# Performance work log

Measured on AMD Instinct MI355X. Metric: run time of the kernel, lower is better.

Reference implementation:

```python
import jax, jax.numpy as jnp
import numpy as np

EMB = 384
H = 6
D = 64  # head_size = EMB // H
FF = 4 * EMB
B, T = 256, 256
EPS = 1e-5


def layernorm(x, g, b):
    mu = jnp.mean(x, axis=-1, keepdims=True)
    var = jnp.var(x, axis=-1, keepdims=True)
    return (x - mu) * jax.lax.rsqrt(var + EPS) * g + b


def setup_inputs() -> dict:
    key = jax.random.key(0)
    ks = jax.random.split(key, 12)
    s_qkv = 1.0 / np.sqrt(EMB)
    return {
        "x":  jax.random.normal(ks[0], (B, T, EMB), jnp.float32),
        # per-head Q/K/V projections stacked: [EMB, H, D]
        "Wq": jax.random.normal(ks[1], (EMB, H, D), jnp.float32) * s_qkv,
        "Wk": jax.random.normal(ks[2], (EMB, H, D), jnp.float32) * s_qkv,
        "Wv": jax.random.normal(ks[3], (EMB, H, D), jnp.float32) * s_qkv,
        "Wo": jax.random.normal(ks[4], (EMB, EMB), jnp.float32) * s_qkv,
        "bo": jnp.zeros((EMB,), jnp.float32),
        "W1": jax.random.normal(ks[5], (EMB, FF), jnp.float32) * s_qkv,
        "b1": jnp.zeros((FF,), jnp.float32),
        "W2": jax.random.normal(ks[6], (FF, EMB), jnp.float32) * (1.0 / np.sqrt(FF)),
        "b2": jnp.zeros((EMB,), jnp.float32),
        "g1": jnp.ones((EMB,), jnp.float32),
        "be1": jnp.zeros((EMB,), jnp.float32),
        "g2": jnp.ones((EMB,), jnp.float32),
        "be2": jnp.zeros((EMB,), jnp.float32),
    }


def reference(x, Wq, Wk, Wv, Wo, bo, W1, b1, W2, b2, g1, be1, g2, be2):
    # pre-LN attention (unmasked encoder block, dropout in eval mode = identity)
    h = layernorm(x, g1, be1)                      # [B,T,C]
    q = jnp.einsum('btc,chd->bhtd', h, Wq)
    k = jnp.einsum('btc,chd->bhtd', h, Wk)
    v = jnp.einsum('btc,chd->bhtd', h, Wv)
    scores = jnp.einsum('bhtd,bhsd->bhts', q, k) * (D ** -0.5)
    attn = jax.nn.softmax(scores, axis=-1)         # [B,H,T,T]
    o = jnp.einsum('bhts,bhsd->bhtd', attn, v)
    o = o.transpose(0, 2, 1, 3).reshape(x.shape[0], x.shape[1], EMB)  # concat heads
    x = x + o @ Wo + bo
    h2 = layernorm(x, g2, be2)
    ff = jax.nn.relu(h2 @ W1 + b1) @ W2 + b2
    return x + ff
```

## Files before the change

### kernel.cpp

```cpp
#include <hip/hip_runtime.h>

typedef __attribute__((ext_vector_type(8))) short bf16x8;
typedef __attribute__((ext_vector_type(4))) float f32x4;
typedef __attribute__((ext_vector_type(4))) unsigned short u16x4;
typedef __attribute__((ext_vector_type(4))) unsigned int u32x4;
typedef __attribute__((ext_vector_type(2))) unsigned int u32x2;

#define DEVFN static __device__ __forceinline__

DEVFN unsigned short f2b(float f) {
  union { float f; unsigned u; } x; x.f = f;
  unsigned r = x.u + 0x7FFFu + ((x.u >> 16) & 1u);
  return (unsigned short)(r >> 16);
}

DEVFN unsigned cvtpk(float lo, float hi) {
  unsigned r;
  asm("v_cvt_pk_bf16_f32 %0, %1, %2" : "=v"(r) : "v"(lo), "v"(hi));
  return r;
}

DEVFN void gll16(const void* g, void* l) {
  __builtin_amdgcn_global_load_lds(
      (const __attribute__((address_space(1))) unsigned int*)g,
      (__attribute__((address_space(3))) unsigned int*)l, 16, 0, 0);
}

#define MFMA16(a, b, c) __builtin_amdgcn_mfma_f32_16x16x32_bf16((a), (b), (c), 0, 0, 0)

__global__ __launch_bounds__(256) void prep_kernel(
    const float* __restrict__ Wq, const float* __restrict__ Wk, const float* __restrict__ Wv,
    const float* __restrict__ Wo, const float* __restrict__ W1, const float* __restrict__ W2,
    short* __restrict__ wqkvT, short* __restrict__ woT,
    short* __restrict__ w1T, short* __restrict__ w2T)
{
  int idx = blockIdx.x * 256 + threadIdx.x;
  if (idx < 442368) {
    int n = idx / 384, kk = idx - n * 384;
    int sec = n / 384, ww = n - sec * 384;
    const float* s = sec == 0 ? Wq : (sec == 1 ? Wk : Wv);
    float sc = (sec == 0) ? 0.125f : 1.0f;
    wqkvT[idx] = (short)f2b(s[kk * 384 + ww] * sc);
  } else if (idx < 589824) {
    int j = idx - 442368;
    int n = j / 384, kk = j - n * 384;
    woT[j] = (short)f2b(Wo[kk * 384 + n]);
  } else if (idx < 1179648) {
    int j = idx - 589824;
    int n = j / 384, kk = j - n * 384;
    w1T[j] = (short)f2b(W1[kk * 1536 + n]);
  } else if (idx < 1769472) {
    int j = idx - 1179648;
    int n = j / 1536, kk = j - n * 1536;
    w2T[j] = (short)f2b(W2[kk * 384 + n]);
  }
}

__global__ __launch_bounds__(256) void ln_kernel(
    const float* __restrict__ x, const float* __restrict__ g, const float* __restrict__ b,
    short* __restrict__ out)
{
  int row = blockIdx.x * 4 + (threadIdx.x >> 6);
  int l = threadIdx.x & 63;
  const float* xr = x + (size_t)row * 384;
  float v[6], s = 0.f, s2 = 0.f;
  #pragma unroll
  for (int i = 0; i < 6; ++i) { v[i] = xr[l + 64 * i]; s += v[i]; s2 += v[i] * v[i]; }
  #pragma unroll
  for (int m = 1; m < 64; m <<= 1) { s += __shfl_xor(s, m); s2 += __shfl_xor(s2, m); }
  float mu = s * (1.f / 384.f);
  float rs = rsqrtf(s2 * (1.f / 384.f) - mu * mu + 1e-5f);
  short* orow = out + (size_t)row * 384;
  #pragma unroll
  for (int i = 0; i < 6; ++i) {
    int c = l + 64 * i;
    orow[c] = (short)f2b((v[i] - mu) * rs * g[c] + b[c]);
  }
}

template<int EPI>
__global__ __launch_bounds__(512) void gemm_bt(
    const short* __restrict__ A, const short* __restrict__ BT,
    int K, int kt, int N, int nx,
    const float* __restrict__ bias, const float* __restrict__ resid,
    float* __restrict__ fout,
    short* __restrict__ qb, short* __restrict__ kb, short* __restrict__ vb)
{
  __shared__ short As[256 * 64];
  __shared__ short Bs[128 * 64];
  const int tid = threadIdx.x;
  const int l = tid & 63, w = tid >> 6;
  const int cl = l & 15, rq = l >> 4;
  const int wr = (w >> 1) * 64, wc = (w & 1) * 64;

  const int nwg = gridDim.x, bid = blockIdx.x;
  const int q8 = nwg >> 3, r8 = nwg & 7;
  const int xcd = bid & 7, ii = bid >> 3;
  const int wg = (xcd < r8) ? xcd * (q8 + 1) + ii : r8 * (q8 + 1) + (xcd - r8) * q8 + ii;
  const int bx = wg % nx, by = wg / nx;

  const int m0 = by * 256, n0 = bx * 128;
  const short* Ab = A + (size_t)m0 * K;
  const short* Bb = BT + (size_t)n0 * K;

  f32x4 acc[4][4] = {};

  for (int ks = 0; ks < kt; ++ks) {
    const int k0 = ks * 64;
    __syncthreads();
    #pragma unroll
    for (int i = 0; i < 4; ++i) {
      int slot = i * 512 + tid;
      int row = slot >> 3, g = slot & 7;
      int gs = g ^ (row & 7);
      gll16(Ab + (size_t)row * K + k0 + gs * 8, &As[slot * 8]);
    }
    #pragma unroll
    for (int i = 0; i < 2; ++i) {
      int slot = i * 512 + tid;
      int row = slot >> 3, g = slot & 7;
      int gs = g ^ (row & 7);
      gll16(Bb + (size_t)row * K + k0 + gs * 8, &Bs[slot * 8]);
    }
    __syncthreads();
    #pragma unroll
    for (int kk = 0; kk < 2; ++kk) {
      bf16x8 af[4], bfr[4];
      #pragma unroll
      for (int m = 0; m < 4; ++m) {
        int row = wr + m * 16 + cl;
        af[m] = *(const bf16x8*)&As[row * 64 + (((kk * 4 + rq) ^ (row & 7)) * 8)];
      }
      #pragma unroll
      for (int n = 0; n < 4; ++n) {
        int row = wc + n * 16 + cl;
        bfr[n] = *(const bf16x8*)&Bs[row * 64 + (((kk * 4 + rq) ^ (row & 7)) * 8)];
      }
      #pragma unroll
      for (int m = 0; m < 4; ++m)
        #pragma unroll
        for (int n = 0; n < 4; ++n)
          acc[m][n] = MFMA16(af[m], bfr[n], acc[m][n]);
    }
  }

  const int gr0 = m0 + wr, gc0 = n0 + wc;
  #pragma unroll
  for (int m = 0; m < 4; ++m) {
    #pragma unroll
    for (int n = 0; n < 4; ++n) {
      int col = gc0 + n * 16 + cl;
      int rbase = gr0 + m * 16 + rq * 4;
      if constexpr (EPI == 0) {
        int sec = col / 384;
        int wcol = col - sec * 384;
        int hh = wcol >> 6, d = wcol & 63;
        int bidx = rbase >> 8, t0 = rbase & 255;
        if (sec == 2) {
          u16x4 pk;
          #pragma unroll
          for (int r = 0; r < 4; ++r) pk[r] = f2b(acc[m][n][r]);
          *(u16x4*)&vb[((size_t)(bidx * 6 + hh) * 64 + d) * 256 + t0] = pk;
        } else {
          short* dst = (sec == 0) ? qb : kb;
          #pragma unroll
          for (int r = 0; r < 4; ++r)
            dst[((size_t)(bidx * 6 + hh) * 256 + t0 + r) * 64 + d] = (short)f2b(acc[m][n][r]);
        }
      } else {
        #pragma unroll
        for (int r = 0; r < 4; ++r) {
          size_t ix = (size_t)(rbase + r) * N + col;
          fout[ix] = acc[m][n][r] + bias[col] + resid[ix];
        }
      }
    }
  }
}

__global__ __launch_bounds__(512, 2) void ff_fused(
    const short* __restrict__ h2,
    const short* __restrict__ w1T,
    const short* __restrict__ w2T,
    const float* __restrict__ b1, const float* __restrict__ b2,
    float* __restrict__ out)
{
  __shared__ short As[128 * 64];
  __shared__ short W1s[128 * 64];
  __shared__ short Acts[128 * 128];
  __shared__ short W2s[384 * 64];
  const int tid = threadIdx.x;
  const int l = tid & 63, w = tid >> 6;
  const int cl = l & 15, rq = l >> 4;
  const int wm = w >> 2, wn = w & 3;
  const int m0 = blockIdx.x * 128;

  f32x4 acc[4][6] = {};

  for (int c = 0; c < 12; ++c) {
    f32x4 aacc[8] = {};
    for (int ks = 0; ks < 6; ++ks) {
      __syncthreads();
      #pragma unroll
      for (int i = 0; i < 2; ++i) {
        int slot = i * 512 + tid;
        int row = slot >> 3, g = slot & 7;
        int gs = g ^ (row & 7);
        gll16(h2 + (size_t)(m0 + row) * 384 + ks * 64 + gs * 8, &As[slot * 8]);
        gll16(w1T + (size_t)(c * 128 + row) * 384 + ks * 64 + gs * 8, &W1s[slot * 8]);
      }
      __syncthreads();
      #pragma unroll
      for (int kk = 0; kk < 2; ++kk) {
        int wrow = w * 16 + cl;
        bf16x8 w1f = *(const bf16x8*)&W1s[wrow * 64 + (((kk * 4 + rq) ^ (wrow & 7)) * 8)];
        #pragma unroll
        for (int m8 = 0; m8 < 8; ++m8) {
          int arow = m8 * 16 + cl;
          bf16x8 hf = *(const bf16x8*)&As[arow * 64 + (((kk * 4 + rq) ^ (arow & 7)) * 8)];
          aacc[m8] = MFMA16(w1f, hf, aacc[m8]);
        }
      }
    }
    f32x4 b1v = *(const f32x4*)&b1[c * 128 + w * 16 + 4 * rq];
    #pragma unroll
    for (int m8 = 0; m8 < 8; ++m8) {
      int row = m8 * 16 + cl;
      int gran = 2 * w + (rq >> 1);
      int off = row * 128 + ((gran ^ (row & 7)) * 8) + ((rq & 1) * 4);
      float v0 = fmaxf(aacc[m8][0] + b1v[0], 0.f);
      float v1 = fmaxf(aacc[m8][1] + b1v[1], 0.f);
      float v2 = fmaxf(aacc[m8][2] + b1v[2], 0.f);
      float v3 = fmaxf(aacc[m8][3] + b1v[3], 0.f);
      u32x2 pw; pw[0] = cvtpk(v0, v1); pw[1] = cvtpk(v2, v3);
      *(u32x2*)&Acts[off] = pw;
    }
    #pragma unroll
    for (int fk = 0; fk < 2; ++fk) {
      __syncthreads();
      #pragma unroll
      for (int i = 0; i < 6; ++i) {
        int slot = i * 512 + tid;
        int row = slot >> 3, g = slot & 7;
        int gs = g ^ (row & 7);
        gll16(w2T + (size_t)row * 1536 + c * 128 + fk * 64 + gs * 8, &W2s[slot * 8]);
      }
      __syncthreads();
      #pragma unroll
      for (int kk = 0; kk < 2; ++kk) {
        bf16x8 af[4], bf[6];
        #pragma unroll
        for (int m = 0; m < 4; ++m) {
          int row = wm * 64 + m * 16 + cl;
          int gran = fk * 8 + kk * 4 + rq;
          af[m] = *(const bf16x8*)&Acts[row * 128 + ((gran ^ (row & 7)) * 8)];
        }
        #pragma unroll
        for (int n = 0; n < 6; ++n) {
          int row = wn * 96 + n * 16 + cl;
          bf[n] = *(const bf16x8*)&W2s[row * 64 + (((kk * 4 + rq) ^ (row & 7)) * 8)];
        }
        #pragma unroll
        for (int m = 0; m < 4; ++m)
          #pragma unroll
          for (int n = 0; n < 6; ++n)
            acc[m][n] = MFMA16(af[m], bf[n], acc[m][n]);
      }
    }
  }
  #pragma unroll
  for (int m = 0; m < 4; ++m) {
    #pragma unroll
    for (int n = 0; n < 6; ++n) {
      int col = wn * 96 + n * 16 + cl;
      int rbase = m0 + wm * 64 + m * 16 + 4 * rq;
      #pragma unroll
      for (int r = 0; r < 4; ++r) {
        size_t ix = (size_t)(rbase + r) * 384 + col;
        out[ix] = acc[m][n][r] + b2[col] + out[ix];
      }
    }
  }
}

__global__ __launch_bounds__(1024) void attn_kernel(
    const short* __restrict__ qg, const short* __restrict__ kg,
    const short* __restrict__ vg, short* __restrict__ og)
{
  __shared__ short Ks[256 * 64];
  __shared__ short Vs[64 * 256];
  const int tid = threadIdx.x;
  const int bh = blockIdx.x;
  const int w = tid >> 6, l = tid & 63;
  const int cl = l & 15, rq = l >> 4;
  const short* kgb = kg + (size_t)bh * 16384;
  const short* vgb = vg + (size_t)bh * 16384;
  #pragma unroll
  for (int i = 0; i < 2; ++i) {
    int slot = i * 1024 + tid;
    int row = slot >> 3, g = slot & 7;
    gll16(kgb + row * 64 + (g ^ (row & 7)) * 8, &Ks[slot * 8]);
  }
  #pragma unroll
  for (int i = 0; i < 2; ++i) {
    int slot = i * 1024 + tid;
    int row = slot >> 5, g = slot & 31;
    int gs = (g & 24) | ((g ^ row) & 7);
    gll16(vgb + row * 256 + gs * 8, &Vs[slot * 8]);
  }
  const int qrow = w * 16 + cl;
  const bf16x8* qp = (const bf16x8*)(qg + ((size_t)bh * 256 + qrow) * 64 + rq * 8);
  bf16x8 qf0 = qp[0], qf1 = qp[4];
  const int b = bh / 6, hh = bh - b * 6;
  __syncthreads();

  f32x4 s[16] = {};
  #pragma unroll
  for (int c = 0; c < 16; ++c) {
    int srow = c * 16 + cl;
    bf16x8 k0 = *(const bf16x8*)&Ks[srow * 64 + ((rq ^ (srow & 7)) * 8)];
    bf16x8 k1 = *(const bf16x8*)&Ks[srow * 64 + (((4 + rq) ^ (srow & 7)) * 8)];
    s[c] = MFMA16(k0, qf0, s[c]);
    s[c] = MFMA16(k1, qf1, s[c]);
  }
  float mr[8];
  #pragma unroll
  for (int c = 0; c < 8; ++c)
    mr[c] = fmaxf(fmaxf(fmaxf(s[2*c][0], s[2*c][1]), fmaxf(s[2*c][2], s[2*c][3])),
                  fmaxf(fmaxf(s[2*c+1][0], s[2*c+1][1]), fmaxf(s[2*c+1][2], s[2*c+1][3])));
  float m = fmaxf(fmaxf(fmaxf(mr[0], mr[1]), fmaxf(mr[2], mr[3])),
                  fmaxf(fmaxf(mr[4], mr[5]), fmaxf(mr[6], mr[7])));
  m = fmaxf(m, __shfl_xor(m, 16));
  m = fmaxf(m, __shfl_xor(m, 32));
  float tc[16];
  #pragma unroll
  for (int c = 0; c < 16; ++c) {
    #pragma unroll
    for (int r = 0; r < 4; ++r) s[c][r] = __expf(s[c][r] - m);
    tc[c] = (s[c][0] + s[c][1]) + (s[c][2] + s[c][3]);
  }
  float t = ((tc[0]+tc[1])+(tc[2]+tc[3])) + ((tc[4]+tc[5])+(tc[6]+tc[7]))
          + ((tc[8]+tc[9])+(tc[10]+tc[11])) + ((tc[12]+tc[13])+(tc[14]+tc[15]));
  t += __shfl_xor(t, 16);
  t += __shfl_xor(t, 32);
  const float inv = 1.f / t;

  f32x4 oacc[4] = {};
  const int idx1 = (((2 * rq) & 3) * 16 + cl) << 2;
  const int idx2 = (((2 * rq + 1) & 3) * 16 + cl) << 2;
  const bool up = rq >= 2;
  #pragma unroll
  for (int ch = 0; ch < 8; ++ch) {
    int X0 = (int)cvtpk(s[2*ch][0], s[2*ch][1]);
    int X1 = (int)cvtpk(s[2*ch][2], s[2*ch][3]);
    int X2 = (int)cvtpk(s[2*ch+1][0], s[2*ch+1][1]);
    int X3 = (int)cvtpk(s[2*ch+1][2], s[2*ch+1][3]);
    int lo0 = __builtin_amdgcn_ds_bpermute(idx1, X0);
    int lo1 = __builtin_amdgcn_ds_bpermute(idx1, X1);
    int hi0 = __builtin_amdgcn_ds_bpermute(idx1, X2);
    int hi1 = __builtin_amdgcn_ds_bpermute(idx1, X3);
    int lo2 = __builtin_amdgcn_ds_bpermute(idx2, X0);
    int lo3 = __builtin_amdgcn_ds_bpermute(idx2, X1);
    int hi2 = __builtin_amdgcn_ds_bpermute(idx2, X2);
    int hi3 = __builtin_amdgcn_ds_bpermute(idx2, X3);
    u32x4 words;
    words[0] = (unsigned)(up ? hi0 : lo0);
    words[1] = (unsigned)(up ? hi1 : lo1);
    words[2] = (unsigned)(up ? hi2 : lo2);
    words[3] = (unsigned)(up ? hi3 : lo3);
    bf16x8 pa = __builtin_bit_cast(bf16x8, words);
    #pragma unroll
    for (int n = 0; n < 4; ++n) {
      int vrow = n * 16 + cl;
      int gg = ch * 4 + rq;
      int gs = (gg & 24) | ((gg ^ vrow) & 7);
      bf16x8 vf = *(const bf16x8*)&Vs[vrow * 256 + gs * 8];
      oacc[n] = MFMA16(pa, vf, oacc[n]);
    }
  }
  float invr[4];
  #pragma unroll
  for (int r = 0; r < 4; ++r) invr[r] = __shfl(inv, 4 * rq + r);
  #pragma unroll
  for (int n = 0; n < 4; ++n) {
    #pragma unroll
    for (int r = 0; r < 4; ++r) {
      int trow = w * 16 + 4 * rq + r;
      og[((size_t)(b * 256 + trow)) * 384 + hh * 64 + n * 16 + cl] =
          (short)f2b(oacc[n][r] * invr[r]);
    }
  }
}

extern "C" void kernel_launch(void* const* d_in, const int* in_sizes, int n_in,
                              void* d_out, int out_size, void* d_ws, size_t ws_size,
                              hipStream_t stream) {
  const float* x   = (const float*)d_in[0];
  const float* Wq  = (const float*)d_in[1];
  const float* Wk  = (const float*)d_in[2];
  const float* Wv  = (const float*)d_in[3];
  const float* Wo  = (const float*)d_in[4];
  const float* bo  = (const float*)d_in[5];
  const float* W1  = (const float*)d_in[6];
  const float* b1  = (const float*)d_in[7];
  const float* W2  = (const float*)d_in[8];
  const float* b2  = (const float*)d_in[9];
  const float* g1  = (const float*)d_in[10];
  const float* be1 = (const float*)d_in[11];
  const float* g2  = (const float*)d_in[12];
  const float* be2 = (const float*)d_in[13];

  char* ws = (char*)d_ws;
  short* wqkvT = (short*)(ws);
  short* woT   = (short*)(ws + 884736);
  short* w1T   = (short*)(ws + 1179648);
  short* w2T   = (short*)(ws + 2359296);
  short* bufA  = (short*)(ws + 3538944);
  short* h  = bufA;
  short* q  = bufA + 25165824;
  short* k  = bufA + 50331648;
  short* v  = bufA + 75497472;
  short* o  = bufA;
  short* h2 = bufA + 25165824;
  float* out = (float*)d_out;

  prep_kernel<<<6912, 256, 0, stream>>>(Wq, Wk, Wv, Wo, W1, W2, wqkvT, woT, w1T, w2T);
  ln_kernel<<<16384, 256, 0, stream>>>(x, g1, be1, h);
  gemm_bt<0><<<9 * 256, 512, 0, stream>>>(h, wqkvT, 384, 6, 1152, 9,
      nullptr, nullptr, nullptr, q, k, v);
  attn_kernel<<<1536, 1024, 0, stream>>>(q, k, v, o);
  gemm_bt<1><<<3 * 256, 512, 0, stream>>>(o, woT, 384, 6, 384, 3,
      bo, x, out, nullptr, nullptr, nullptr);
  ln_kernel<<<16384, 256, 0, stream>>>(out, g2, be2, h2);
  ff_fused<<<512, 512, 0, stream>>>(h2, w1T, w2T, b1, b2, out);
}
```

Baseline: 583.5 us.

## Restructure fused FFN: 64-row tiles, resident activations in LDS, weights from global

```diff
diff --git a/kernel.cpp b/kernel.cpp
--- a/kernel.cpp
+++ b/kernel.cpp
@@ -178,102 +178,92 @@
   }
 }
 
-__global__ __launch_bounds__(512, 2) void ff_fused(
+__global__ __launch_bounds__(512, 4) void ff_fused(
     const short* __restrict__ h2,
     const short* __restrict__ w1T,
     const short* __restrict__ w2T,
     const float* __restrict__ b1, const float* __restrict__ b2,
     float* __restrict__ out)
 {
-  __shared__ short As[128 * 64];
-  __shared__ short W1s[128 * 64];
-  __shared__ short Acts[128 * 128];
-  __shared__ short W2s[384 * 64];
+  __shared__ short As[64 * 384];
+  __shared__ short Acts[64 * 128];
   const int tid = threadIdx.x;
   const int l = tid & 63, w = tid >> 6;
   const int cl = l & 15, rq = l >> 4;
   const int wm = w >> 2, wn = w & 3;
-  const int m0 = blockIdx.x * 128;
-
-  f32x4 acc[4][6] = {};
+  const int m0 = blockIdx.x * 64;
+
+  #pragma unroll
+  for (int i = 0; i < 6; ++i) {
+    int slot = i * 512 + tid;
+    int row = slot / 48, g = slot - row * 48;
+    int gs = (g & 56) | ((g ^ row) & 7);
+    gll16(h2 + (size_t)(m0 + row) * 384 + gs * 8, &As[slot * 8]);
+  }
+  __syncthreads();
+
+  f32x4 acc[2][6] = {};
 
   for (int c = 0; c < 12; ++c) {
-    f32x4 aacc[8] = {};
+    f32x4 aacc[4] = {};
+    const short* w1p = w1T + (size_t)(c * 128 + w * 16 + cl) * 384;
+    #pragma unroll
     for (int ks = 0; ks < 6; ++ks) {
-      __syncthreads();
-      #pragma unroll
-      for (int i = 0; i < 2; ++i) {
-        int slot = i * 512 + tid;
-        int row = slot >> 3, g = slot & 7;
-        int gs = g ^ (row & 7);
-        gll16(h2 + (size_t)(m0 + row) * 384 + ks * 64 + gs * 8, &As[slot * 8]);
-        gll16(w1T + (size_t)(c * 128 + row) * 384 + ks * 64 + gs * 8, &W1s[slot * 8]);
-      }
-      __syncthreads();
       #pragma unroll
       for (int kk = 0; kk < 2; ++kk) {
-        int wrow = w * 16 + cl;
-        bf16x8 w1f = *(const bf16x8*)&W1s[wrow * 64 + (((kk * 4 + rq) ^ (wrow & 7)) * 8)];
-        #pragma unroll
-        for (int m8 = 0; m8 < 8; ++m8) {
+        bf16x8 w1f = *(const bf16x8*)&w1p[ks * 64 + (kk * 4 + rq) * 8];
+        int gran = ks * 8 + kk * 4 + rq;
+        #pragma unroll
+        for (int m8 = 0; m8 < 4; ++m8) {
           int arow = m8 * 16 + cl;
-          bf16x8 hf = *(const bf16x8*)&As[arow * 64 + (((kk * 4 + rq) ^ (arow & 7)) * 8)];
+          bf16x8 hf = *(const bf16x8*)&As[arow * 384 +
+              (((gran & 56) | ((gran ^ arow) & 7)) * 8)];
           aacc[m8] = MFMA16(w1f, hf, aacc[m8]);
         }
       }
     }
+    __syncthreads();
     f32x4 b1v = *(const f32x4*)&b1[c * 128 + w * 16 + 4 * rq];
     #pragma unroll
-    for (int m8 = 0; m8 < 8; ++m8) {
+    for (int m8 = 0; m8 < 4; ++m8) {
       int row = m8 * 16 + cl;
-      int gran = 2 * w + (rq >> 1);
-      int off = row * 128 + ((gran ^ (row & 7)) * 8) + ((rq & 1) * 4);
-      float v0 = fmaxf(aacc[m8][0] + b1v[0], 0.f);
-      float v1 = fmaxf(aacc[m8][1] + b1v[1], 0.f);
-      float v2 = fmaxf(aacc[m8][2] + b1v[2], 0.f);
-      float v3 = fmaxf(aacc[m8][3] + b1v[3], 0.f);
-      u32x2 pw; pw[0] = cvtpk(v0, v1); pw[1] = cvtpk(v2, v3);
+      int gran2 = 2 * w + (rq >> 1);
+      int off = row * 128 + ((gran2 ^ (row & 7)) * 8) + ((rq & 1) * 4);
+      u32x2 pw;
+      pw[0] = cvtpk(fmaxf(aacc[m8][0] + b1v[0], 0.f), fmaxf(aacc[m8][1] + b1v[1], 0.f));
+      pw[1] = cvtpk(fmaxf(aacc[m8][2] + b1v[2], 0.f), fmaxf(aacc[m8][3] + b1v[3], 0.f));
       *(u32x2*)&Acts[off] = pw;
     }
+    __syncthreads();
     #pragma unroll
     for (int fk = 0; fk < 2; ++fk) {
-      __syncthreads();
-      #pragma unroll
-      for (int i = 0; i < 6; ++i) {
-        int slot = i * 512 + tid;
-        int row = slot >> 3, g = slot & 7;
-        int gs = g ^ (row & 7);
-        gll16(w2T + (size_t)row * 1536 + c * 128 + fk * 64 + gs * 8, &W2s[slot * 8]);
-      }
-      __syncthreads();
       #pragma unroll
       for (int kk = 0; kk < 2; ++kk) {
-        bf16x8 af[4], bf[6];
-        #pragma unroll
-        for (int m = 0; m < 4; ++m) {
-          int row = wm * 64 + m * 16 + cl;
-          int gran = fk * 8 + kk * 4 + rq;
+        int gran = fk * 8 + kk * 4 + rq;
+        bf16x8 af[2], bfr[6];
+        #pragma unroll
+        for (int m = 0; m < 2; ++m) {
+          int row = wm * 32 + m * 16 + cl;
           af[m] = *(const bf16x8*)&Acts[row * 128 + ((gran ^ (row & 7)) * 8)];
         }
         #pragma unroll
-        for (int n = 0; n < 6; ++n) {
-          int row = wn * 96 + n * 16 + cl;
-          bf[n] = *(const bf16x8*)&W2s[row * 64 + (((kk * 4 + rq) ^ (row & 7)) * 8)];
-        }
-        #pragma unroll
-        for (int m = 0; m < 4; ++m)
+        for (int n = 0; n < 6; ++n)
+          bfr[n] = *(const bf16x8*)&w2T[(size_t)(wn * 96 + n * 16 + cl) * 1536 +
+                                        c * 128 + fk * 64 + (kk * 4 + rq) * 8];
+        #pragma unroll
+        for (int m = 0; m < 2; ++m)
           #pragma unroll
           for (int n = 0; n < 6; ++n)
-            acc[m][n] = MFMA16(af[m], bf[n], acc[m][n]);
-      }
-    }
-  }
-  #pragma unroll
-  for (int m = 0; m < 4; ++m) {
+            acc[m][n] = MFMA16(af[m], bfr[n], acc[m][n]);
+      }
+    }
+  }
+  #pragma unroll
+  for (int m = 0; m < 2; ++m) {
     #pragma unroll
     for (int n = 0; n < 6; ++n) {
       int col = wn * 96 + n * 16 + cl;
-      int rbase = m0 + wm * 64 + m * 16 + 4 * rq;
+      int rbase = m0 + wm * 32 + m * 16 + 4 * rq;
       #pragma unroll
       for (int r = 0; r < 4; ++r) {
         size_t ix = (size_t)(rbase + r) * 384 + col;
@@ -432,5 +422,5 @@
   gemm_bt<1><<<3 * 256, 512, 0, stream>>>(o, woT, 384, 6, 384, 3,
       bo, x, out, nullptr, nullptr, nullptr);
   ln_kernel<<<16384, 256, 0, stream>>>(out, g2, be2, h2);
-  ff_fused<<<512, 512, 0, stream>>>(h2, w1T, w2T, b1, b2, out);
-}
+  ff_fused<<<1024, 512, 0, stream>>>(h2, w1T, w2T, b1, b2, out);
+}
```

Result: slower. 727.2 us (+24.6%).

## Fuse Wo projection with LayerNorm2 and split FFN into chunked GEMMs

Applied to the files above, without the earlier changes.

```diff
diff --git a/kernel.cpp b/kernel.cpp
--- a/kernel.cpp
+++ b/kernel.cpp
@@ -4,7 +4,6 @@
 typedef __attribute__((ext_vector_type(4))) float f32x4;
 typedef __attribute__((ext_vector_type(4))) unsigned short u16x4;
 typedef __attribute__((ext_vector_type(4))) unsigned int u32x4;
-typedef __attribute__((ext_vector_type(2))) unsigned int u32x2;
 
 #define DEVFN static __device__ __forceinline__
 
@@ -83,7 +82,7 @@
     const short* __restrict__ A, const short* __restrict__ BT,
     int K, int kt, int N, int nx,
     const float* __restrict__ bias, const float* __restrict__ resid,
-    float* __restrict__ fout,
+    float* __restrict__ fout, short* __restrict__ bout,
     short* __restrict__ qb, short* __restrict__ kb, short* __restrict__ vb)
 {
   __shared__ short As[256 * 64];
@@ -167,117 +166,127 @@
           for (int r = 0; r < 4; ++r)
             dst[((size_t)(bidx * 6 + hh) * 256 + t0 + r) * 64 + d] = (short)f2b(acc[m][n][r]);
         }
-      } else {
+      } else if constexpr (EPI == 1) {
         #pragma unroll
         for (int r = 0; r < 4; ++r) {
           size_t ix = (size_t)(rbase + r) * N + col;
           fout[ix] = acc[m][n][r] + bias[col] + resid[ix];
         }
-      }
-    }
-  }
-}
-
-__global__ __launch_bounds__(512, 2) void ff_fused(
-    const short* __restrict__ h2,
-    const short* __restrict__ w1T,
-    const short* __restrict__ w2T,
-    const float* __restrict__ b1, const float* __restrict__ b2,
-    float* __restrict__ out)
+      } else {
+        #pragma unroll
+        for (int r = 0; r < 4; ++r)
+          bout[(size_t)(rbase + r) * N + col] = (short)f2b(fmaxf(acc[m][n][r] + bias[col], 0.f));
+      }
+    }
+  }
+}
+
+__global__ __launch_bounds__(512) void wo_ln_kernel(
+    const short* __restrict__ A,
+    const short* __restrict__ BT,
+    const float* __restrict__ bo, const float* __restrict__ x,
+    const float* __restrict__ g2, const float* __restrict__ be2,
+    float* __restrict__ out, short* __restrict__ h2)
 {
   __shared__ short As[128 * 64];
-  __shared__ short W1s[128 * 64];
-  __shared__ short Acts[128 * 128];
-  __shared__ short W2s[384 * 64];
+  __shared__ short Bs[384 * 64];
+  __shared__ float redS[128][4], redQ[128][4];
+  __shared__ float redMu[128], redRs[128];
   const int tid = threadIdx.x;
   const int l = tid & 63, w = tid >> 6;
   const int cl = l & 15, rq = l >> 4;
   const int wm = w >> 2, wn = w & 3;
-  const int m0 = blockIdx.x * 128;
+
+  const int nwg = gridDim.x, bid = blockIdx.x;
+  const int q8 = nwg >> 3;
+  const int wg = (bid & 7) * q8 + (bid >> 3);
+  const int m0 = wg * 128;
+  const short* Ab = A + (size_t)m0 * 384;
 
   f32x4 acc[4][6] = {};
 
-  for (int c = 0; c < 12; ++c) {
-    f32x4 aacc[8] = {};
-    for (int ks = 0; ks < 6; ++ks) {
-      __syncthreads();
-      #pragma unroll
-      for (int i = 0; i < 2; ++i) {
-        int slot = i * 512 + tid;
-        int row = slot >> 3, g = slot & 7;
-        int gs = g ^ (row & 7);
-        gll16(h2 + (size_t)(m0 + row) * 384 + ks * 64 + gs * 8, &As[slot * 8]);
-        gll16(w1T + (size_t)(c * 128 + row) * 384 + ks * 64 + gs * 8, &W1s[slot * 8]);
-      }
-      __syncthreads();
-      #pragma unroll
-      for (int kk = 0; kk < 2; ++kk) {
-        int wrow = w * 16 + cl;
-        bf16x8 w1f = *(const bf16x8*)&W1s[wrow * 64 + (((kk * 4 + rq) ^ (wrow & 7)) * 8)];
+  for (int ks = 0; ks < 6; ++ks) {
+    const int k0 = ks * 64;
+    __syncthreads();
+    #pragma unroll
+    for (int i = 0; i < 2; ++i) {
+      int slot = i * 512 + tid;
+      int row = slot >> 3, g = slot & 7;
+      int gs = g ^ (row & 7);
+      gll16(Ab + (size_t)row * 384 + k0 + gs * 8, &As[slot * 8]);
+    }
+    #pragma unroll
+    for (int i = 0; i < 6; ++i) {
+      int slot = i * 512 + tid;
+      int row = slot >> 3, g = slot & 7;
+      int gs = g ^ (row & 7);
+      gll16(BT + (size_t)row * 384 + k0 + gs * 8, &Bs[slot * 8]);
+    }
+    __syncthreads();
+    #pragma unroll
+    for (int kk = 0; kk < 2; ++kk) {
+      bf16x8 af[4], bfr[6];
+      #pragma unroll
+      for (int m = 0; m < 4; ++m) {
+        int row = wm * 64 + m * 16 + cl;
+        af[m] = *(const bf16x8*)&As[row * 64 + (((kk * 4 + rq) ^ (row & 7)) * 8)];
+      }
+      #pragma unroll
+      for (int n = 0; n < 6; ++n) {
+        int row = wn * 96 + n * 16 + cl;
+        bfr[n] = *(const bf16x8*)&Bs[row * 64 + (((kk * 4 + rq) ^ (row & 7)) * 8)];
+      }
+      #pragma unroll
+      for (int m = 0; m < 4; ++m)
         #pragma unroll
-        for (int m8 = 0; m8 < 8; ++m8) {
-          int arow = m8 * 16 + cl;
-          bf16x8 hf = *(const bf16x8*)&As[arow * 64 + (((kk * 4 + rq) ^ (arow & 7)) * 8)];
-          aacc[m8] = MFMA16(w1f, hf, aacc[m8]);
-        }
-      }
-    }
-    f32x4 b1v = *(const f32x4*)&b1[c * 128 + w * 16 + 4 * rq];
-    #pragma unroll
-    for (int m8 = 0; m8 < 8; ++m8) {
-      int row = m8 * 16 + cl;
-      int gran = 2 * w + (rq >> 1);
-      int off = row * 128 + ((gran ^ (row & 7)) * 8) + ((rq & 1) * 4);
-      float v0 = fmaxf(aacc[m8][0] + b1v[0], 0.f);
-      float v1 = fmaxf(aacc[m8][1] + b1v[1], 0.f);
-      float v2 = fmaxf(aacc[m8][2] + b1v[2], 0.f);
-      float v3 = fmaxf(aacc[m8][3] + b1v[3], 0.f);
-      u32x2 pw; pw[0] = cvtpk(v0, v1); pw[1] = cvtpk(v2, v3);
-      *(u32x2*)&Acts[off] = pw;
-    }
-    #pragma unroll
-    for (int fk = 0; fk < 2; ++fk) {
-      __syncthreads();
-      #pragma unroll
-      for (int i = 0; i < 6; ++i) {
-        int slot = i * 512 + tid;
-        int row = slot >> 3, g = slot & 7;
-        int gs = g ^ (row & 7);
-        gll16(w2T + (size_t)row * 1536 + c * 128 + fk * 64 + gs * 8, &W2s[slot * 8]);
-      }
-      __syncthreads();
-      #pragma unroll
-      for (int kk = 0; kk < 2; ++kk) {
-        bf16x8 af[4], bf[6];
-        #pragma unroll
-        for (int m = 0; m < 4; ++m) {
-          int row = wm * 64 + m * 16 + cl;
-          int gran = fk * 8 + kk * 4 + rq;
-          af[m] = *(const bf16x8*)&Acts[row * 128 + ((gran ^ (row & 7)) * 8)];
-        }
-        #pragma unroll
-        for (int n = 0; n < 6; ++n) {
-          int row = wn * 96 + n * 16 + cl;
-          bf[n] = *(const bf16x8*)&W2s[row * 64 + (((kk * 4 + rq) ^ (row & 7)) * 8)];
-        }
-        #pragma unroll
-        for (int m = 0; m < 4; ++m)
-          #pragma unroll
-          for (int n = 0; n < 6; ++n)
-            acc[m][n] = MFMA16(af[m], bf[n], acc[m][n]);
-      }
-    }
-  }
+        for (int n = 0; n < 6; ++n)
+          acc[m][n] = MFMA16(af[m], bfr[n], acc[m][n]);
+    }
+  }
+
   #pragma unroll
   for (int m = 0; m < 4; ++m) {
     #pragma unroll
-    for (int n = 0; n < 6; ++n) {
-      int col = wn * 96 + n * 16 + cl;
-      int rbase = m0 + wm * 64 + m * 16 + 4 * rq;
-      #pragma unroll
-      for (int r = 0; r < 4; ++r) {
-        size_t ix = (size_t)(rbase + r) * 384 + col;
-        out[ix] = acc[m][n][r] + b2[col] + out[ix];
+    for (int r = 0; r < 4; ++r) {
+      int lrow = wm * 64 + m * 16 + rq * 4 + r;
+      float p = 0.f, qs = 0.f;
+      #pragma unroll
+      for (int n = 0; n < 6; ++n) {
+        int col = wn * 96 + n * 16 + cl;
+        size_t ix = (size_t)(m0 + lrow) * 384 + col;
+        float v = acc[m][n][r] + bo[col] + x[ix];
+        acc[m][n][r] = v;
+        out[ix] = v;
+        p += v; qs += v * v;
+      }
+      #pragma unroll
+      for (int msk = 1; msk < 16; msk <<= 1) {
+        p += __shfl_xor(p, msk);
+        qs += __shfl_xor(qs, msk);
+      }
+      if (cl == 0) { redS[lrow][wn] = p; redQ[lrow][wn] = qs; }
+    }
+  }
+  __syncthreads();
+  if (tid < 128) {
+    float S = redS[tid][0] + redS[tid][1] + redS[tid][2] + redS[tid][3];
+    float Q = redQ[tid][0] + redQ[tid][1] + redQ[tid][2] + redQ[tid][3];
+    float mu = S * (1.f / 384.f);
+    redMu[tid] = mu;
+    redRs[tid] = rsqrtf(Q * (1.f / 384.f) - mu * mu + 1e-5f);
+  }
+  __syncthreads();
+  #pragma unroll
+  for (int m = 0; m < 4; ++m) {
+    #pragma unroll
+    for (int r = 0; r < 4; ++r) {
+      int lrow = wm * 64 + m * 16 + rq * 4 + r;
+      float mu = redMu[lrow], rs = redRs[lrow];
+      #pragma unroll
+      for (int n = 0; n < 6; ++n) {
+        int col = wn * 96 + n * 16 + cl;
+        h2[(size_t)(m0 + lrow) * 384 + col] =
+            (short)f2b((acc[m][n][r] - mu) * rs * g2[col] + be2[col]);
       }
     }
   }
@@ -422,15 +431,20 @@
   short* v  = bufA + 75497472;
   short* o  = bufA;
   short* h2 = bufA + 25165824;
+  short* act = bufA + 50331648;
   float* out = (float*)d_out;
 
   prep_kernel<<<6912, 256, 0, stream>>>(Wq, Wk, Wv, Wo, W1, W2, wqkvT, woT, w1T, w2T);
   ln_kernel<<<16384, 256, 0, stream>>>(x, g1, be1, h);
   gemm_bt<0><<<9 * 256, 512, 0, stream>>>(h, wqkvT, 384, 6, 1152, 9,
-      nullptr, nullptr, nullptr, q, k, v);
+      nullptr, nullptr, nullptr, nullptr, q, k, v);
   attn_kernel<<<1536, 1024, 0, stream>>>(q, k, v, o);
-  gemm_bt<1><<<3 * 256, 512, 0, stream>>>(o, woT, 384, 6, 384, 3,
-      bo, x, out, nullptr, nullptr, nullptr);
-  ln_kernel<<<16384, 256, 0, stream>>>(out, g2, be2, h2);
-  ff_fused<<<512, 512, 0, stream>>>(h2, w1T, w2T, b1, b2, out);
-}
+  wo_ln_kernel<<<512, 512, 0, stream>>>(o, woT, bo, x, g2, be2, out, h2);
+  for (int c = 0; c < 2; ++c) {
+    const size_t roff = (size_t)c * 32768 * 384;
+    gemm_bt<2><<<12 * 128, 512, 0, stream>>>(h2 + roff, w1T, 384, 6, 1536, 12,
+        b1, nullptr, nullptr, act, nullptr, nullptr, nullptr);
+    gemm_bt<1><<<3 * 128, 512, 0, stream>>>(act, w2T, 1536, 24, 384, 3,
+        b2, out + roff, out + roff, nullptr, nullptr, nullptr, nullptr);
+  }
+}
```

New measurement: 514.9 us. 1.13x faster.
